# Performance work log

Hardware: AMD Instinct MI355X
Metric: run time of the kernel (lower is better)

The kernel has to match this reference:

```python
import jax, jax.numpy as jnp
import numpy as np

N = 10000      # nodes
E = 160000     # edges (before self loops)
F_IN = 512     # in_features
F_OUT = 256    # out_features
SLOPE = 0.2    # LeakyReLU negative slope (PyG GATConv default)
EPS = 1e-12    # F.normalize eps


def setup_inputs() -> dict:
    key = jax.random.key(0)
    ks = jax.random.split(key, 14)
    feat = jax.random.normal(ks[0], (N, F_IN), jnp.float32)
    feat_a = jax.random.normal(ks[1], (N, F_IN), jnp.float32)
    edge_index = jax.random.randint(ks[2], (2, E), 0, N, dtype=jnp.int32)
    # binary neighborhood mask; diagonal set so every row has >=1 entry
    gn = (jax.random.uniform(ks[3], (N, N)) < 0.0016).astype(jnp.float32)
    graph_neigh = gn.at[jnp.arange(N), jnp.arange(N)].set(1.0)
    s1 = 1.0 / np.sqrt(F_IN)
    s2 = 1.0 / np.sqrt(F_OUT)
    return {
        "feat": feat,
        "feat_a": feat_a,
        "edge_index": edge_index,
        "graph_neigh": graph_neigh,
        # conv1: GATConv(F_IN -> F_OUT, heads=1)
        "W1": jax.random.normal(ks[4], (F_OUT, F_IN), jnp.float32) * s1,
        "att_src1": jax.random.normal(ks[5], (F_OUT,), jnp.float32) * s2,
        "att_dst1": jax.random.normal(ks[6], (F_OUT,), jnp.float32) * s2,
        "b1": jnp.zeros((F_OUT,), jnp.float32),
        # conv2: GATConv(F_OUT -> F_IN, heads=1)
        "W2": jax.random.normal(ks[7], (F_IN, F_OUT), jnp.float32) * s2,
        "att_src2": jax.random.normal(ks[8], (F_IN,), jnp.float32) * s1,
        "att_dst2": jax.random.normal(ks[9], (F_IN,), jnp.float32) * s1,
        "b2": jnp.zeros((F_IN,), jnp.float32),
        # discriminator bilinear
        "Wd": jax.random.normal(ks[10], (F_OUT, F_OUT), jnp.float32) * s2,
        "bd": jnp.zeros((), jnp.float32),
    }


def _gat_conv(x, src, dst, W, a_src, a_dst, b):
    # PyG GATConv, heads=1, concat=True, add_self_loops already applied.
    h = x @ W.T                       # [N, out]
    a_s = h @ a_src                   # [N]
    a_d = h @ a_dst                   # [N]
    e = a_s[src] + a_d[dst]           # [E+N]
    e = jnp.where(e > 0, e, SLOPE * e)  # leaky relu
    m = jax.ops.segment_max(e, dst, num_segments=N)
    p = jnp.exp(e - m[dst])
    s = jax.ops.segment_sum(p, dst, num_segments=N)
    coef = p / s[dst]                 # per-dst softmax over incoming edges
    out = jax.ops.segment_sum(coef[:, None] * h[src], dst, num_segments=N)
    return out + b


def reference(feat, feat_a, edge_index, graph_neigh, W1, att_src1, att_dst1, b1,
              W2, att_src2, att_dst2, b2, Wd, bd):
    loops = jnp.arange(N, dtype=edge_index.dtype)
    src = jnp.concatenate([edge_index[0], loops])
    dst = jnp.concatenate([edge_index[1], loops])

    z = _gat_conv(feat, src, dst, W1, att_src1, att_dst1, b1)      # [N, F_OUT]
    hiden_emb = z
    h = _gat_conv(z, src, dst, W2, att_src2, att_dst2, b2)         # [N, F_IN]
    emb = jax.nn.relu(z)
    z_a = _gat_conv(feat_a, src, dst, W1, att_src1, att_dst1, b1)
    emb_a = jax.nn.relu(z_a)

    def readout(e):
        vsum = graph_neigh @ e                                     # [N, F_OUT]
        row_sum = graph_neigh.sum(axis=1, keepdims=True)
        g = vsum / row_sum
        g = g / jnp.maximum(jnp.linalg.norm(g, axis=1, keepdims=True), EPS)
        return jax.nn.sigmoid(g)

    g = readout(emb)
    g_a = readout(emb_a)

    def bilin(x1, x2):
        return jnp.einsum('nd,de,ne->n', x1, Wd, x2)[:, None] + bd

    ret = jnp.concatenate([bilin(emb, g), bilin(emb_a, g)], axis=1)      # [N, 2]
    ret_a = jnp.concatenate([bilin(emb_a, g_a), bilin(emb, g_a)], axis=1)
    return (hiden_emb, h, ret, ret_a)
```

## Files before the change

### kernel.cpp

```cpp
#include <hip/hip_runtime.h>


#define N_NODES 10000
#define F_IN    512
#define F_OUT   256
#define SLOPE   0.2f
#define BCAP    64

typedef unsigned short ushort_t;
typedef __attribute__((ext_vector_type(8))) short short8;
typedef __attribute__((ext_vector_type(4))) float f32x4;

__device__ __forceinline__ float bf2f(ushort_t h) {
    union { unsigned u; float f; } v;
    v.u = ((unsigned)h) << 16;
    return v.f;
}
__device__ __forceinline__ ushort_t f2bf(float f) {
    union { float f; unsigned u; } v; v.f = f;
    unsigned r = v.u + 0x7FFFu + ((v.u >> 16) & 1u);
    return (ushort_t)(r >> 16);
}

#define NF (N_NODES * 512)
#define NW1 (512 * 256)
#define NW2 (512 * 256)
#define NWD (256 * 256)

__global__ __launch_bounds__(256) void cvt_all(const float* __restrict__ feat,
                                               const float* __restrict__ feat_a,
                                               const float* __restrict__ W1,
                                               const float* __restrict__ W2,
                                               const float* __restrict__ Wd,
                                               ushort_t* __restrict__ featbf,
                                               ushort_t* __restrict__ W1bf,
                                               ushort_t* __restrict__ W2bf,
                                               ushort_t* __restrict__ Wdbf,
                                               uint4* __restrict__ zbase, int zu4) {
    int q = blockIdx.x * 256 + threadIdx.x;
    const int total = (2 * NF + NW1 + NW2 + NWD) / 4;
    if (q >= total) {
        int zi = q - total;
        if (zi < zu4) zbase[zi] = make_uint4(0, 0, 0, 0);
        return;
    }
    int i = q * 4;
    const float* s; ushort_t* d;
    if (i < NF)               { s = feat   + i;                 d = featbf + i; }
    else if (i < 2 * NF)      { s = feat_a + (i - NF);          d = featbf + i; }
    else if (i < 2 * NF + NW1){ s = W1 + (i - 2 * NF);          d = W1bf + (i - 2 * NF); }
    else if (i < 2 * NF + NW1 + NW2) { s = W2 + (i - 2 * NF - NW1); d = W2bf + (i - 2 * NF - NW1); }
    else                      { s = Wd + (i - 2 * NF - NW1 - NW2); d = Wdbf + (i - 2 * NF - NW1 - NW2); }
    float4 v = *(const float4*)s;
    uint2 r;
    r.x = (unsigned)f2bf(v.x) | ((unsigned)f2bf(v.y) << 16);
    r.y = (unsigned)f2bf(v.z) | ((unsigned)f2bf(v.w) << 16);
    *(uint2*)d = r;
}

__global__ void bucket_fill(const int* __restrict__ src, const int* __restrict__ dst,
                            int E, int n, int* cnt, int* buckets) {
    int i = blockIdx.x * 256 + threadIdx.x;
    if (i < E) {
        int d = dst[i];
        d = d < 0 ? 0 : (d >= n ? n - 1 : d);
        int s = src[i];
        s = s < 0 ? 0 : (s >= n ? n - 1 : s);
        int p = atomicAdd(&cnt[d], 1);
        if (p < BCAP) buckets[d * BCAP + p] = s;
    } else if (i < E + n) {
        int v = i - E;
        int p = atomicAdd(&cnt[v], 1);
        if (p < BCAP) buckets[v * BCAP + p] = v;
    }
}

#define BM 64
#define BN 64
#define BK 32

__global__ __launch_bounds__(256) void gemm_bt(const ushort_t* __restrict__ A,
                                               const ushort_t* __restrict__ B,
                                               ushort_t* __restrict__ C,
                                               int M, int N, int K,
                                               const float* __restrict__ asrc,
                                               const float* __restrict__ adst,
                                               float* __restrict__ as_out,
                                               float* __restrict__ ad_out) {
    __shared__ __align__(16) ushort_t As[BM * BK];
    __shared__ __align__(16) ushort_t Bs[BN * BK];
    int m0 = blockIdx.x * BM;
    int n0 = blockIdx.y * BN;
    int tid = threadIdx.x;
    int wave = tid >> 6, lane = tid & 63;
    int quad = lane >> 4, r16 = lane & 15;

    f32x4 acc[4] = {};

    int srow = tid >> 2;
    int schunk = tid & 3;
    int a_row = m0 + srow; if (a_row >= M) a_row = M - 1;
    const uint4* Ag = (const uint4*)(A + (size_t)a_row * K);
    const uint4* Bg = (const uint4*)(B + (size_t)(n0 + srow) * K);
    int s_sw = srow * BK + ((schunk ^ (srow & 3)) * 8);

    for (int k0 = 0; k0 < K; k0 += BK) {
        uint4 av = Ag[(k0 >> 3) + schunk];
        uint4 bv = Bg[(k0 >> 3) + schunk];
        __syncthreads();
        *(uint4*)&As[s_sw] = av;
        *(uint4*)&Bs[s_sw] = bv;
        __syncthreads();
        int am = wave * 16 + r16;
        short8 a = *(const short8*)&As[am * BK + ((quad ^ (am & 3)) * 8)];
#pragma unroll
        for (int i = 0; i < 4; i++) {
            int bn = i * 16 + r16;
            short8 b = *(const short8*)&Bs[bn * BK + ((quad ^ (bn & 3)) * 8)];
            acc[i] = __builtin_amdgcn_mfma_f32_16x16x32_bf16(a, b, acc[i], 0, 0, 0);
        }
    }
    int m_base = m0 + wave * 16 + quad * 4;
#pragma unroll
    for (int i = 0; i < 4; i++) {
        int n = n0 + i * 16 + r16;
#pragma unroll
        for (int r = 0; r < 4; r++) {
            int m = m_base + r;
            if (m < M) C[(size_t)m * N + n] = f2bf(acc[i][r]);
        }
    }
    if (as_out) {
        float a0 = asrc[n0 + r16],      d0 = adst[n0 + r16];
        float a1 = asrc[n0 + 16 + r16], d1 = adst[n0 + 16 + r16];
        float a2 = asrc[n0 + 32 + r16], d2 = adst[n0 + 32 + r16];
        float a3 = asrc[n0 + 48 + r16], d3 = adst[n0 + 48 + r16];
#pragma unroll
        for (int r = 0; r < 4; r++) {
            float s  = acc[0][r] * a0 + acc[1][r] * a1 + acc[2][r] * a2 + acc[3][r] * a3;
            float dd = acc[0][r] * d0 + acc[1][r] * d1 + acc[2][r] * d2 + acc[3][r] * d3;
#pragma unroll
            for (int off = 1; off < 16; off <<= 1) {
                s  += __shfl_xor(s, off);
                dd += __shfl_xor(dd, off);
            }
            int m = m_base + r;
            if (r16 == 0 && m < M) {
                atomicAdd(&as_out[m], s);
                atomicAdd(&ad_out[m], dd);
            }
        }
    }
}

template<int NV>
__device__ __forceinline__ void accum_row(float wgt, const ushort_t* p, float* acc) {
    if constexpr (NV == 4) {
        uint2 u = *(const uint2*)p;
        acc[0] += wgt * bf2f((ushort_t)(u.x & 0xFFFFu));
        acc[1] += wgt * bf2f((ushort_t)(u.x >> 16));
        acc[2] += wgt * bf2f((ushort_t)(u.y & 0xFFFFu));
        acc[3] += wgt * bf2f((ushort_t)(u.y >> 16));
    } else {
        uint4 u = *(const uint4*)p;
        acc[0] += wgt * bf2f((ushort_t)(u.x & 0xFFFFu));
        acc[1] += wgt * bf2f((ushort_t)(u.x >> 16));
        acc[2] += wgt * bf2f((ushort_t)(u.y & 0xFFFFu));
        acc[3] += wgt * bf2f((ushort_t)(u.y >> 16));
        acc[4] += wgt * bf2f((ushort_t)(u.z & 0xFFFFu));
        acc[5] += wgt * bf2f((ushort_t)(u.z >> 16));
        acc[6] += wgt * bf2f((ushort_t)(u.w & 0xFFFFu));
        acc[7] += wgt * bf2f((ushort_t)(u.w >> 16));
    }
}

template<int NV>
__device__ __forceinline__ void store_bf(ushort_t* dst, const float* z, bool relu) {
    unsigned rp[NV / 2];
#pragma unroll
    for (int k = 0; k < NV; k += 2) {
        float x = relu ? fmaxf(z[k], 0.f) : z[k];
        float y = relu ? fmaxf(z[k + 1], 0.f) : z[k + 1];
        rp[k / 2] = (unsigned)f2bf(x) | ((unsigned)f2bf(y) << 16);
    }
    if constexpr (NV == 4) {
        *(uint2*)dst = make_uint2(rp[0], rp[1]);
    } else {
        *(uint4*)dst = make_uint4(rp[0], rp[1], rp[2], rp[3]);
    }
}

template<int FF>
__global__ __launch_bounds__(256) void row_conv_w(const int* __restrict__ cnt,
                                                  const int* __restrict__ buckets,
                                                  const float* __restrict__ a_s,
                                                  const float* __restrict__ a_d,
                                                  const ushort_t* __restrict__ h,
                                                  const float* __restrict__ bias,
                                                  int nfirst, int ntot,
                                                  float* __restrict__ out0,
                                                  ushort_t* __restrict__ outZ,
                                                  ushort_t* __restrict__ outB,
                                                  ushort_t* __restrict__ out1) {
    constexpr int NV = FF / 64;
    int w = blockIdx.x * 4 + (threadIdx.x >> 6);
    if (w >= ntot) return;
    int lane = threadIdx.x & 63;
    int sel = (w >= nfirst) ? 1 : 0;
    int n = w - sel * nfirst;
    size_t roff = (size_t)sel * (size_t)nfirst;
    int deg = min(cnt[n], BCAP);
    float adn = a_d[roff + n];

    float acc[NV];
#pragma unroll
    for (int k = 0; k < NV; k++) acc[k] = 0.f;

    int cv = 0; float e = -1e30f;
    if (lane < deg) {
        cv = buckets[n * BCAP + lane];
        float t = a_s[roff + cv] + adn;
        e = t > 0.f ? t : SLOPE * t;
    }
    float m = e;
#pragma unroll
    for (int off = 32; off; off >>= 1) m = fmaxf(m, __shfl_xor(m, off));
    float wv = (lane < deg) ? expf(e - m) : 0.f;
    float ls = wv;
#pragma unroll
    for (int off = 32; off; off >>= 1) ls += __shfl_xor(ls, off);
    float inv_s = ls > 0.f ? 1.f / ls : 0.f;
    int j = 0;
    for (; j + 3 < deg; j += 4) {
        float w0 = __shfl(wv, j),     w1 = __shfl(wv, j + 1);
        float w2 = __shfl(wv, j + 2), w3 = __shfl(wv, j + 3);
        int   q0 = __shfl(cv, j),     q1 = __shfl(cv, j + 1);
        int   q2 = __shfl(cv, j + 2), q3 = __shfl(cv, j + 3);
        accum_row<NV>(w0, h + (size_t)(roff + q0) * FF + lane * NV, acc);
        accum_row<NV>(w1, h + (size_t)(roff + q1) * FF + lane * NV, acc);
        accum_row<NV>(w2, h + (size_t)(roff + q2) * FF + lane * NV, acc);
        accum_row<NV>(w3, h + (size_t)(roff + q3) * FF + lane * NV, acc);
    }
    for (; j < deg; j++) {
        float wj = __shfl(wv, j);
        int   qj = __shfl(cv, j);
        accum_row<NV>(wj, h + (size_t)(roff + qj) * FF + lane * NV, acc);
    }

    float z[NV];
#pragma unroll
    for (int k = 0; k < NV; k++) z[k] = acc[k] * inv_s + bias[lane * NV + k];

    size_t obase = (size_t)n * FF + lane * NV;
    if (sel == 0) {
        if (out0) {
#pragma unroll
            for (int k = 0; k < NV; k += 4)
                *(float4*)(out0 + obase + k) = make_float4(z[k], z[k+1], z[k+2], z[k+3]);
        }
        if (outZ) store_bf<NV>(outZ + obase, z, false);
        if (outB) store_bf<NV>(outB + obase, z, true);
    } else {
        if (out1) store_bf<NV>(out1 + obase, z, true);
    }
}

#define RCAP 256

__global__ __launch_bounds__(256) void readout_w(const float* __restrict__ gn,
                                                 const ushort_t* __restrict__ embB,
                                                 const ushort_t* __restrict__ embA,
                                                 ushort_t* __restrict__ g,
                                                 ushort_t* __restrict__ ga) {
    int wid = threadIdx.x >> 6, lane = threadIdx.x & 63;
    int n = blockIdx.x * 4 + wid;
    __shared__ int lists[4][RCAP];
    __shared__ int cnts[4];
    if (lane == 0) cnts[wid] = 0;
    __syncthreads();
    const uint4* rowp = (const uint4*)(gn + (size_t)n * N_NODES);
    const int NU4 = N_NODES / 4;
    for (int idx = lane; idx < NU4; idx += 64) {
        uint4 v = rowp[idx];
        if (v.x & 0x7FFFFFFFu) { int p = atomicAdd(&cnts[wid], 1); if (p < RCAP) lists[wid][p] = idx * 4; }
        if (v.y & 0x7FFFFFFFu) { int p = atomicAdd(&cnts[wid], 1); if (p < RCAP) lists[wid][p] = idx * 4 + 1; }
        if (v.z & 0x7FFFFFFFu) { int p = atomicAdd(&cnts[wid], 1); if (p < RCAP) lists[wid][p] = idx * 4 + 2; }
        if (v.w & 0x7FFFFFFFu) { int p = atomicAdd(&cnts[wid], 1); if (p < RCAP) lists[wid][p] = idx * 4 + 3; }
    }
    __syncthreads();
    int c = min(cnts[wid], RCAP);
    float a0[4] = {}, a1[4] = {};
    int j = 0;
    for (; j + 3 < c; j += 4) {
        int i0 = lists[wid][j],     i1 = lists[wid][j + 1];
        int i2 = lists[wid][j + 2], i3 = lists[wid][j + 3];
        accum_row<4>(1.f, embB + (size_t)i0 * 256 + lane * 4, a0);
        accum_row<4>(1.f, embB + (size_t)i1 * 256 + lane * 4, a0);
        accum_row<4>(1.f, embB + (size_t)i2 * 256 + lane * 4, a0);
        accum_row<4>(1.f, embB + (size_t)i3 * 256 + lane * 4, a0);
        accum_row<4>(1.f, embA + (size_t)i0 * 256 + lane * 4, a1);
        accum_row<4>(1.f, embA + (size_t)i1 * 256 + lane * 4, a1);
        accum_row<4>(1.f, embA + (size_t)i2 * 256 + lane * 4, a1);
        accum_row<4>(1.f, embA + (size_t)i3 * 256 + lane * 4, a1);
    }
    for (; j < c; j++) {
        int node = lists[wid][j];
        accum_row<4>(1.f, embB + (size_t)node * 256 + lane * 4, a0);
        accum_row<4>(1.f, embA + (size_t)node * 256 + lane * 4, a1);
    }
    float inv = 1.f / (float)(c > 0 ? c : 1);
    float u0[4], u1[4];
    float s0 = 0.f, s1 = 0.f;
#pragma unroll
    for (int k = 0; k < 4; k++) {
        u0[k] = a0[k] * inv; s0 += u0[k] * u0[k];
        u1[k] = a1[k] * inv; s1 += u1[k] * u1[k];
    }
#pragma unroll
    for (int off = 32; off; off >>= 1) {
        s0 += __shfl_xor(s0, off);
        s1 += __shfl_xor(s1, off);
    }
    float r0 = 1.f / fmaxf(sqrtf(s0), 1e-12f);
    float r1 = 1.f / fmaxf(sqrtf(s1), 1e-12f);
    float go[4], gao[4];
#pragma unroll
    for (int k = 0; k < 4; k++) {
        go[k]  = 1.f / (1.f + expf(-u0[k] * r0));
        gao[k] = 1.f / (1.f + expf(-u1[k] * r1));
    }
    store_bf<4>(g  + (size_t)n * 256 + lane * 4, go,  false);
    store_bf<4>(ga + (size_t)n * 256 + lane * 4, gao, false);
}

__global__ __launch_bounds__(256) void bilin_kernel(const float* __restrict__ z,
                                                    const ushort_t* __restrict__ embA,
                                                    const ushort_t* __restrict__ Q,
                                                    const ushort_t* __restrict__ Qa,
                                                    const float* __restrict__ bdp,
                                                    float* __restrict__ ret,
                                                    float* __restrict__ ret_a) {
    int row = blockIdx.x * 4 + (threadIdx.x >> 6);
    int lane = threadIdx.x & 63;
    if (row >= N_NODES) return;
    const float*    zr = z    + (size_t)row * 256;
    const ushort_t* er = embA + (size_t)row * 256;
    const ushort_t* q  = Q    + (size_t)row * 256;
    const ushort_t* qa = Qa   + (size_t)row * 256;
    float d00 = 0, d01 = 0, d10 = 0, d11 = 0;
    for (int d = lane; d < 256; d += 64) {
        float em = fmaxf(zr[d], 0.f);
        float ea = bf2f(er[d]);
        float qv = bf2f(q[d]), qav = bf2f(qa[d]);
        d00 += em * qv;
        d01 += ea * qv;
        d10 += ea * qav;
        d11 += em * qav;
    }
    for (int off = 32; off; off >>= 1) {
        d00 += __shfl_down(d00, off);
        d01 += __shfl_down(d01, off);
        d10 += __shfl_down(d10, off);
        d11 += __shfl_down(d11, off);
    }
    if (lane == 0) {
        float bd = bdp[0];
        ret[row * 2]       = d00 + bd;
        ret[row * 2 + 1]   = d01 + bd;
        ret_a[row * 2]     = d10 + bd;
        ret_a[row * 2 + 1] = d11 + bd;
    }
}

extern "C" void kernel_launch(void* const* d_in, const int* in_sizes, int n_in,
                              void* d_out, int out_size, void* d_ws, size_t ws_size,
                              hipStream_t stream) {
    const float* feat    = (const float*)d_in[0];
    const float* feat_a  = (const float*)d_in[1];
    const int*   eidx    = (const int*)d_in[2];
    const float* gn      = (const float*)d_in[3];
    const float* W1      = (const float*)d_in[4];
    const float* asrc1   = (const float*)d_in[5];
    const float* adst1   = (const float*)d_in[6];
    const float* b1      = (const float*)d_in[7];
    const float* W2      = (const float*)d_in[8];
    const float* asrc2   = (const float*)d_in[9];
    const float* adst2   = (const float*)d_in[10];
    const float* b2      = (const float*)d_in[11];
    const float* Wd      = (const float*)d_in[12];
    const float* bd      = (const float*)d_in[13];

    const int N = N_NODES;
    const int E = in_sizes[2] / 2;
    const int* src = eidx;
    const int* dst = eidx + E;

    float* out_z    = (float*)d_out;
    float* out_h    = out_z + (size_t)N * F_OUT;
    float* out_ret  = out_h + (size_t)N * F_IN;
    float* out_reta = out_ret + (size_t)N * 2;

    size_t off = 0;
    char* wsb = (char*)d_ws;
    auto carve = [&](size_t bytes) -> void* {
        void* p = wsb + off;
        off = (off + bytes + 255) & ~(size_t)255;
        return p;
    };
    ushort_t* R1     = (ushort_t*)carve((size_t)2 * N * 256 * 2);
    ushort_t* R2     = (ushort_t*)carve((size_t)2 * N * 256 * 2);
    ushort_t* embA   = (ushort_t*)carve((size_t)N * 256 * 2);
    ushort_t* embB   = (ushort_t*)carve((size_t)N * 256 * 2);
    ushort_t* zbf    = (ushort_t*)carve((size_t)N * 256 * 2);
    ushort_t* featbf = (ushort_t*)carve((size_t)2 * N * 512 * 2);
    ushort_t* W1bf   = (ushort_t*)carve((size_t)NW1 * 2);
    ushort_t* W2bf   = (ushort_t*)carve((size_t)NW2 * 2);
    ushort_t* Wdbf   = (ushort_t*)carve((size_t)NWD * 2);
    size_t zstart = off;
    float* as1cat = (float*)carve((size_t)2 * N * 4);
    float* ad1cat = (float*)carve((size_t)2 * N * 4);
    float* as2    = (float*)carve((size_t)N * 4);
    float* ad2    = (float*)carve((size_t)N * 4);
    int*   cnt    = (int*)carve((size_t)N * 4);
    size_t zend = off;
    int*   buckets = (int*)carve((size_t)N * BCAP * 4);

    ushort_t* h1cat = R1;
    ushort_t* h2    = R1;
    ushort_t* gbuf  = R1;
    ushort_t* gabuf = R1 + (size_t)N * 256;
    ushort_t* Qb    = R2;
    ushort_t* Qab   = R2 + (size_t)N * 256;

    const int cvt_total = (2 * NF + NW1 + NW2 + NWD) / 4;
    const int zu4 = (int)((zend - zstart) / 16);
    cvt_all<<<(cvt_total + zu4 + 255) / 256, 256, 0, stream>>>(
        feat, feat_a, W1, W2, Wd, featbf, W1bf, W2bf, Wdbf,
        (uint4*)(wsb + zstart), zu4);

    bucket_fill<<<(E + N + 255) / 256, 256, 0, stream>>>(src, dst, E, N, cnt, buckets);

    const int MT  = (N + BM - 1) / BM;
    const int MT2 = (2 * N + BM - 1) / BM;

    gemm_bt<<<dim3(MT2, F_OUT / BN), 256, 0, stream>>>(featbf, W1bf, h1cat,
                                                       2 * N, F_OUT, F_IN,
                                                       asrc1, adst1, as1cat, ad1cat);
    row_conv_w<256><<<2 * N / 4, 256, 0, stream>>>(cnt, buckets, as1cat, ad1cat, h1cat, b1,
                                                   N, 2 * N, out_z, zbf, embB, embA);

    gemm_bt<<<dim3(MT, F_IN / BN), 256, 0, stream>>>(zbf, W2bf, h2,
                                                     N, F_IN, F_OUT,
                                                     asrc2, adst2, as2, ad2);
    row_conv_w<512><<<N / 4, 256, 0, stream>>>(cnt, buckets, as2, ad2, h2, b2,
                                               N, N, out_h, nullptr, nullptr, nullptr);

    readout_w<<<N / 4, 256, 0, stream>>>(gn, embB, embA, gbuf, gabuf);

    gemm_bt<<<dim3(MT2, 256 / BN), 256, 0, stream>>>(R1, Wdbf, R2, 2 * N, 256, 256,
                                                     nullptr, nullptr, nullptr, nullptr);
    bilin_kernel<<<(N + 3) / 4, 256, 0, stream>>>(out_z, embA, Qb, Qab, bd, out_ret, out_reta);
}
```

Measured before the change: 705.7 us.

## Merge independent stages into combined launches via block-range dispatch

Measured after the change: 683.3 us. 1.03x faster.

```diff
diff --git a/kernel.cpp b/kernel.cpp
--- a/kernel.cpp
+++ b/kernel.cpp
@@ -58,39 +58,20 @@
     *(uint2*)d = r;
 }
 
-__global__ void bucket_fill(const int* __restrict__ src, const int* __restrict__ dst,
-                            int E, int n, int* cnt, int* buckets) {
-    int i = blockIdx.x * 256 + threadIdx.x;
-    if (i < E) {
-        int d = dst[i];
-        d = d < 0 ? 0 : (d >= n ? n - 1 : d);
-        int s = src[i];
-        s = s < 0 ? 0 : (s >= n ? n - 1 : s);
-        int p = atomicAdd(&cnt[d], 1);
-        if (p < BCAP) buckets[d * BCAP + p] = s;
-    } else if (i < E + n) {
-        int v = i - E;
-        int p = atomicAdd(&cnt[v], 1);
-        if (p < BCAP) buckets[v * BCAP + p] = v;
-    }
-}
-
 #define BM 64
 #define BN 64
 #define BK 32
-
-__global__ __launch_bounds__(256) void gemm_bt(const ushort_t* __restrict__ A,
-                                               const ushort_t* __restrict__ B,
-                                               ushort_t* __restrict__ C,
-                                               int M, int N, int K,
-                                               const float* __restrict__ asrc,
-                                               const float* __restrict__ adst,
-                                               float* __restrict__ as_out,
-                                               float* __restrict__ ad_out) {
-    __shared__ __align__(16) ushort_t As[BM * BK];
-    __shared__ __align__(16) ushort_t Bs[BN * BK];
-    int m0 = blockIdx.x * BM;
-    int n0 = blockIdx.y * BN;
+#define MT1 157
+#define MT2 313
+
+__device__ __forceinline__ void gemm_bt_dev(ushort_t* As, ushort_t* Bs,
+        int bx, int by,
+        const ushort_t* __restrict__ A, const ushort_t* __restrict__ B,
+        ushort_t* __restrict__ C, int M, int Nn, int K,
+        const float* __restrict__ asrc, const float* __restrict__ adst,
+        float* __restrict__ as_out, float* __restrict__ ad_out) {
+    int m0 = bx * BM;
+    int n0 = by * BN;
     int tid = threadIdx.x;
     int wave = tid >> 6, lane = tid & 63;
     int quad = lane >> 4, r16 = lane & 15;
@@ -127,7 +108,7 @@
 #pragma unroll
         for (int r = 0; r < 4; r++) {
             int m = m_base + r;
-            if (m < M) C[(size_t)m * N + n] = f2bf(acc[i][r]);
+            if (m < M) C[(size_t)m * Nn + n] = f2bf(acc[i][r]);
         }
     }
     if (as_out) {
@@ -191,20 +172,14 @@
 }
 
 template<int FF>
-__global__ __launch_bounds__(256) void row_conv_w(const int* __restrict__ cnt,
-                                                  const int* __restrict__ buckets,
-                                                  const float* __restrict__ a_s,
-                                                  const float* __restrict__ a_d,
-                                                  const ushort_t* __restrict__ h,
-                                                  const float* __restrict__ bias,
-                                                  int nfirst, int ntot,
-                                                  float* __restrict__ out0,
-                                                  ushort_t* __restrict__ outZ,
-                                                  ushort_t* __restrict__ outB,
-                                                  ushort_t* __restrict__ out1) {
+__device__ __forceinline__ void row_conv_dev(int w,
+        const int* __restrict__ cnt, const int* __restrict__ buckets,
+        const float* __restrict__ a_s, const float* __restrict__ a_d,
+        const ushort_t* __restrict__ h, const float* __restrict__ bias,
+        int nfirst,
+        float* __restrict__ out0, ushort_t* __restrict__ outZ,
+        ushort_t* __restrict__ outB, ushort_t* __restrict__ out1) {
     constexpr int NV = FF / 64;
-    int w = blockIdx.x * 4 + (threadIdx.x >> 6);
-    if (w >= ntot) return;
     int lane = threadIdx.x & 63;
     int sel = (w >= nfirst) ? 1 : 0;
     int n = w - sel * nfirst;
@@ -265,17 +240,33 @@
     }
 }
 
+template<int FF>
+__global__ __launch_bounds__(256) void row_conv_w(const int* __restrict__ cnt,
+                                                  const int* __restrict__ buckets,
+                                                  const float* __restrict__ a_s,
+                                                  const float* __restrict__ a_d,
+                                                  const ushort_t* __restrict__ h,
+                                                  const float* __restrict__ bias,
+                                                  int nfirst, int ntot,
+                                                  float* __restrict__ out0,
+                                                  ushort_t* __restrict__ outZ,
+                                                  ushort_t* __restrict__ outB,
+                                                  ushort_t* __restrict__ out1) {
+    int w = blockIdx.x * 4 + (threadIdx.x >> 6);
+    if (w >= ntot) return;
+    row_conv_dev<FF>(w, cnt, buckets, a_s, a_d, h, bias, nfirst, out0, outZ, outB, out1);
+}
+
 #define RCAP 256
 
-__global__ __launch_bounds__(256) void readout_w(const float* __restrict__ gn,
-                                                 const ushort_t* __restrict__ embB,
-                                                 const ushort_t* __restrict__ embA,
-                                                 ushort_t* __restrict__ g,
-                                                 ushort_t* __restrict__ ga) {
+__device__ __forceinline__ void readout_dev(int nbase, char* smemraw,
+        const float* __restrict__ gn,
+        const ushort_t* __restrict__ embB, const ushort_t* __restrict__ embA,
+        ushort_t* __restrict__ g, ushort_t* __restrict__ ga) {
     int wid = threadIdx.x >> 6, lane = threadIdx.x & 63;
-    int n = blockIdx.x * 4 + wid;
-    __shared__ int lists[4][RCAP];
-    __shared__ int cnts[4];
+    int n = nbase + wid;
+    int (*lists)[RCAP] = (int(*)[RCAP])smemraw;
+    int* cnts = (int*)(smemraw + 4 * RCAP * 4);
     if (lane == 0) cnts[wid] = 0;
     __syncthreads();
     const uint4* rowp = (const uint4*)(gn + (size_t)n * N_NODES);
@@ -331,6 +322,91 @@
     }
     store_bf<4>(g  + (size_t)n * 256 + lane * 4, go,  false);
     store_bf<4>(ga + (size_t)n * 256 + lane * 4, gao, false);
+}
+
+#define G1B (MT2 * 4)
+
+__global__ __launch_bounds__(256) void k_conv1(const ushort_t* __restrict__ featbf,
+                                               const ushort_t* __restrict__ W1bf,
+                                               ushort_t* __restrict__ h1cat,
+                                               const float* __restrict__ asrc1,
+                                               const float* __restrict__ adst1,
+                                               float* __restrict__ as1cat,
+                                               float* __restrict__ ad1cat,
+                                               const int* __restrict__ src,
+                                               const int* __restrict__ dst,
+                                               int E, int* cnt, int* buckets) {
+    __shared__ __align__(16) ushort_t As[BM * BK];
+    __shared__ __align__(16) ushort_t Bs[BN * BK];
+    int b = blockIdx.x;
+    if (b < G1B) {
+        gemm_bt_dev(As, Bs, b % MT2, b / MT2, featbf, W1bf, h1cat,
+                    2 * N_NODES, F_OUT, F_IN, asrc1, adst1, as1cat, ad1cat);
+    } else {
+        int i = (b - G1B) * 256 + (int)threadIdx.x;
+        if (i < E) {
+            int d = dst[i];
+            d = d < 0 ? 0 : (d >= N_NODES ? N_NODES - 1 : d);
+            int s = src[i];
+            s = s < 0 ? 0 : (s >= N_NODES ? N_NODES - 1 : s);
+            int p = atomicAdd(&cnt[d], 1);
+            if (p < BCAP) buckets[d * BCAP + p] = s;
+        } else if (i < E + N_NODES) {
+            int v = i - E;
+            int p = atomicAdd(&cnt[v], 1);
+            if (p < BCAP) buckets[v * BCAP + p] = v;
+        }
+    }
+}
+
+#define RO_BLOCKS 2500
+#define G2B (MT1 * 8)
+
+__global__ __launch_bounds__(256) void k_stage2(const ushort_t* __restrict__ zbf,
+                                                const ushort_t* __restrict__ W2bf,
+                                                ushort_t* __restrict__ h2,
+                                                const float* __restrict__ asrc2,
+                                                const float* __restrict__ adst2,
+                                                float* __restrict__ as2,
+                                                float* __restrict__ ad2,
+                                                const float* __restrict__ gn,
+                                                const ushort_t* __restrict__ embB,
+                                                const ushort_t* __restrict__ embA,
+                                                ushort_t* __restrict__ g,
+                                                ushort_t* __restrict__ ga) {
+    __shared__ __align__(16) char smem[2 * BM * BK * 2];
+    int b = blockIdx.x;
+    if (b < RO_BLOCKS) {
+        readout_dev(b * 4, smem, gn, embB, embA, g, ga);
+    } else {
+        int bb = b - RO_BLOCKS;
+        gemm_bt_dev((ushort_t*)smem, (ushort_t*)smem + BM * BK, bb % MT1, bb / MT1,
+                    zbf, W2bf, h2, N_NODES, F_IN, F_OUT, asrc2, adst2, as2, ad2);
+    }
+}
+
+__global__ __launch_bounds__(256) void k_stage3(const int* __restrict__ cnt,
+                                                const int* __restrict__ buckets,
+                                                const float* __restrict__ as2,
+                                                const float* __restrict__ ad2,
+                                                const ushort_t* __restrict__ h2,
+                                                const float* __restrict__ b2,
+                                                float* __restrict__ out_h,
+                                                const ushort_t* __restrict__ Gcat,
+                                                const ushort_t* __restrict__ Wdbf,
+                                                ushort_t* __restrict__ R2) {
+    __shared__ __align__(16) ushort_t As[BM * BK];
+    __shared__ __align__(16) ushort_t Bs[BN * BK];
+    int b = blockIdx.x;
+    if (b < RO_BLOCKS) {
+        int w = b * 4 + ((int)threadIdx.x >> 6);
+        row_conv_dev<512>(w, cnt, buckets, as2, ad2, h2, b2, N_NODES,
+                          out_h, nullptr, nullptr, nullptr);
+    } else {
+        int bb = b - RO_BLOCKS;
+        gemm_bt_dev(As, Bs, bb % MT2, bb / MT2, Gcat, Wdbf, R2,
+                    2 * N_NODES, 256, 256, nullptr, nullptr, nullptr, nullptr);
+    }
 }
 
 __global__ __launch_bounds__(256) void bilin_kernel(const float* __restrict__ z,
@@ -409,6 +485,7 @@
     };
     ushort_t* R1     = (ushort_t*)carve((size_t)2 * N * 256 * 2);
     ushort_t* R2     = (ushort_t*)carve((size_t)2 * N * 256 * 2);
+    ushort_t* Gcat   = (ushort_t*)carve((size_t)2 * N * 256 * 2);
     ushort_t* embA   = (ushort_t*)carve((size_t)N * 256 * 2);
     ushort_t* embB   = (ushort_t*)carve((size_t)N * 256 * 2);
     ushort_t* zbf    = (ushort_t*)carve((size_t)N * 256 * 2);
@@ -427,8 +504,6 @@
 
     ushort_t* h1cat = R1;
     ushort_t* h2    = R1;
-    ushort_t* gbuf  = R1;
-    ushort_t* gabuf = R1 + (size_t)N * 256;
     ushort_t* Qb    = R2;
     ushort_t* Qab   = R2 + (size_t)N * 256;
 
@@ -438,26 +513,19 @@
         feat, feat_a, W1, W2, Wd, featbf, W1bf, W2bf, Wdbf,
         (uint4*)(wsb + zstart), zu4);
 
-    bucket_fill<<<(E + N + 255) / 256, 256, 0, stream>>>(src, dst, E, N, cnt, buckets);
-
-    const int MT  = (N + BM - 1) / BM;
-    const int MT2 = (2 * N + BM - 1) / BM;
-
-    gemm_bt<<<dim3(MT2, F_OUT / BN), 256, 0, stream>>>(featbf, W1bf, h1cat,
-                                                       2 * N, F_OUT, F_IN,
-                                                       asrc1, adst1, as1cat, ad1cat);
+    const int bucketBlocks = (E + N + 255) / 256;
+    k_conv1<<<G1B + bucketBlocks, 256, 0, stream>>>(featbf, W1bf, h1cat,
+                                                    asrc1, adst1, as1cat, ad1cat,
+                                                    src, dst, E, cnt, buckets);
+
     row_conv_w<256><<<2 * N / 4, 256, 0, stream>>>(cnt, buckets, as1cat, ad1cat, h1cat, b1,
                                                    N, 2 * N, out_z, zbf, embB, embA);
 
-    gemm_bt<<<dim3(MT, F_IN / BN), 256, 0, stream>>>(zbf, W2bf, h2,
-                                                     N, F_IN, F_OUT,
-                                                     asrc2, adst2, as2, ad2);
-    row_conv_w<512><<<N / 4, 256, 0, stream>>>(cnt, buckets, as2, ad2, h2, b2,
-                                               N, N, out_h, nullptr, nullptr, nullptr);
-
-    readout_w<<<N / 4, 256, 0, stream>>>(gn, embB, embA, gbuf, gabuf);
-
-    gemm_bt<<<dim3(MT2, 256 / BN), 256, 0, stream>>>(R1, Wdbf, R2, 2 * N, 256, 256,
-                                                     nullptr, nullptr, nullptr, nullptr);
+    k_stage2<<<RO_BLOCKS + G2B, 256, 0, stream>>>(zbf, W2bf, h2, asrc2, adst2, as2, ad2,
+                                                  gn, embB, embA, Gcat, Gcat + (size_t)N * 256);
+
+    k_stage3<<<RO_BLOCKS + G1B, 256, 0, stream>>>(cnt, buckets, as2, ad2, h2, b2, out_h,
+                                                  Gcat, Wdbf, R2);
+
     bilin_kernel<<<(N + 3) / 4, 256, 0, stream>>>(out_z, embA, Qb, Qab, bd, out_ret, out_reta);
 }
```
